# Kernel optimization log

Hardware: AMD Instinct MI355X
Metric: run time of the kernel (lower is better)

The kernel has to match this reference:

```python
import jax, jax.numpy as jnp
import numpy as np
import math

HIDDEN = 1024
HEADS = 16
HEAD_DIM = HIDDEN // HEADS


def setup_inputs() -> dict:
    key = jax.random.key(0)
    ks = jax.random.split(key, 9)
    s = 1.0 / math.sqrt(HIDDEN)
    x = jax.random.normal(ks[0], (4, 2048, HIDDEN), dtype=jnp.float32)
    Wq = jax.random.uniform(ks[1], (HIDDEN, HIDDEN), jnp.float32, -s, s)
    bq = jax.random.uniform(ks[2], (HIDDEN,), jnp.float32, -s, s)
    Wk = jax.random.uniform(ks[3], (HIDDEN, HIDDEN), jnp.float32, -s, s)
    bk = jax.random.uniform(ks[4], (HIDDEN,), jnp.float32, -s, s)
    Wv = jax.random.uniform(ks[5], (HIDDEN, HIDDEN), jnp.float32, -s, s)
    bv = jax.random.uniform(ks[6], (HIDDEN,), jnp.float32, -s, s)
    Wo = jax.random.uniform(ks[7], (HIDDEN, HIDDEN), jnp.float32, -s, s)
    bo = jax.random.uniform(ks[8], (HIDDEN,), jnp.float32, -s, s)
    return {"x": x, "Wq": Wq, "bq": bq, "Wk": Wk, "bk": bk,
            "Wv": Wv, "bv": bv, "Wo": Wo, "bo": bo}


def reference(x, Wq, bq, Wk, bk, Wv, bv, Wo, bo):
    B, T, D = x.shape
    H, Hd = HEADS, HEAD_DIM
    scale = 1.0 / math.sqrt(Hd)
    # projections (torch Linear: y = x @ W.T + b)
    q = (x @ Wq.T + bq).reshape(B, T, H, Hd).transpose(0, 2, 1, 3)  # [B,H,T,Hd]
    k = (x @ Wk.T + bk).reshape(B, T, H, Hd).transpose(0, 2, 1, 3)
    v = (x @ Wv.T + bv).reshape(B, T, H, Hd).transpose(0, 2, 1, 3)
    scores = jnp.einsum("bhqd,bhkd->bhqk", q, k) * scale  # [B,H,T,T]
    attn = jax.nn.softmax(scores, axis=-1)
    out = jnp.einsum("bhqk,bhkd->bhqd", attn, v)  # [B,H,T,Hd]
    out = out.transpose(0, 2, 1, 3).reshape(B, T, D)
    out = out @ Wo.T + bo
    return out.mean(axis=1)  # [B, D]
```

## Files before the change

kernel.cpp:

```cpp
#include <hip/hip_runtime.h>
#include <stdint.h>

#define HIDDEN 1024
#define HEADS 16
#define HEAD_DIM 64
#define BATCH 4
#define SEQ 2048
#define NTOK (BATCH * SEQ)

typedef __attribute__((ext_vector_type(8))) short bf16x8;
typedef __attribute__((ext_vector_type(4))) float floatx4;
typedef __attribute__((ext_vector_type(16))) float floatx16;

#define SCALE_Q 0.18033688011112042f

__device__ __forceinline__ unsigned short f2bf(float f) {
    union { float f; unsigned u; } x; x.f = f;
    unsigned r = x.u + 0x7fffu + ((x.u >> 16) & 1u);
    return (unsigned short)(r >> 16);
}

__device__ __forceinline__ float fast_exp2(float x) {
#if __has_builtin(__builtin_amdgcn_exp2f)
    return __builtin_amdgcn_exp2f(x);
#else
    return exp2f(x);
#endif
}

typedef __attribute__((address_space(3))) unsigned int lds_u32;
typedef const __attribute__((address_space(1))) unsigned int gl_u32;

__device__ __forceinline__ void async_cp16(const void* g, void* l) {
#if __has_builtin(__builtin_amdgcn_global_load_lds)
    __builtin_amdgcn_global_load_lds((gl_u32*)g, (lds_u32*)l, 16, 0, 0);
#else
    *(uint4*)((char*)l + (threadIdx.x & 63) * 16) = *(const uint4*)g;
#endif
}

__global__ __launch_bounds__(256) void conv_all(
    const float* __restrict__ x, const float* __restrict__ Wq,
    const float* __restrict__ Wk, const float* __restrict__ Wv,
    unsigned short* __restrict__ x_bf, unsigned short* __restrict__ wq_bf,
    unsigned short* __restrict__ wk_bf, unsigned short* __restrict__ wv_bf,
    float* __restrict__ accp) {
    const int blk = blockIdx.x, tid = threadIdx.x;
    const float* src;
    unsigned short* dst;
    size_t i;
    if (blk < 8192) {
        src = x; dst = x_bf; i = (size_t)blk * 256 + tid;
        if (blk < 16) accp[blk * 256 + tid] = 0.0f;
    } else {
        int r = blk - 8192;
        int s = r >> 10;
        src = (s == 0) ? Wq : (s == 1) ? Wk : Wv;
        dst = (s == 0) ? wq_bf : (s == 1) ? wk_bf : wv_bf;
        i = (size_t)(r & 1023) * 256 + tid;
    }
    float4 v = *(const float4*)(src + 4 * i);
    unsigned short o[4];
    o[0] = f2bf(v.x); o[1] = f2bf(v.y); o[2] = f2bf(v.z); o[3] = f2bf(v.w);
    *(ushort4*)(dst + 4 * i) = *(ushort4*)o;
}

__global__ __launch_bounds__(256, 2) void qkv_gemm(
    const unsigned short* __restrict__ X,
    const unsigned short* __restrict__ W0, const unsigned short* __restrict__ W1,
    const unsigned short* __restrict__ W2,
    const float* __restrict__ b0, const float* __restrict__ b1,
    const float* __restrict__ b2,
    unsigned short* __restrict__ O0, unsigned short* __restrict__ O1,
    unsigned short* __restrict__ O2) {
    __shared__ unsigned short Alds[2][4096];
    __shared__ unsigned short Blds[2][6144];

    const int id = blockIdx.x;
    const int mb = id & 63, nb = id >> 6;
    const int m0 = mb * 128, n0 = nb * 64;

    const int tid = threadIdx.x, lane = tid & 63, wave = tid >> 6;

    const unsigned short* WZ0 = W0;
    const unsigned short* WZ1 = W1;
    const unsigned short* WZ2 = W2;

    const unsigned short* ga[2];
#pragma unroll
    for (int j = 0; j < 2; ++j)
        ga[j] = X + (size_t)(m0 + wave * 32 + j * 16 + (lane >> 2)) * HIDDEN + (lane & 3) * 8;

    const unsigned short* gb[3];
    int bdst[3];
#pragma unroll
    for (int jj = 0; jj < 3; ++jj) {
        const int i = wave * 3 + jj;
        const int z = i >> 2, seg = i & 3;
        const unsigned short* Wz = (z == 0) ? WZ0 : (z == 1) ? WZ1 : WZ2;
        gb[jj] = Wz + (size_t)(n0 + seg * 16 + (lane >> 2)) * HIDDEN + (lane & 3) * 8;
        bdst[jj] = z * 4096 + seg * 1024;
    }

    floatx4 acc[3][2][4];
#pragma unroll
    for (int z = 0; z < 3; ++z)
#pragma unroll
        for (int tm = 0; tm < 2; ++tm)
#pragma unroll
            for (int tn = 0; tn < 4; ++tn)
#pragma unroll
                for (int r = 0; r < 4; ++r) acc[z][tm][tn][r] = 0.f;

#pragma unroll
    for (int j = 0; j < 2; ++j) {
        async_cp16(ga[j], (char*)Alds[0] + wave * 2048 + j * 1024);
        ga[j] += 32;
    }
#pragma unroll
    for (int jj = 0; jj < 3; ++jj) {
        async_cp16(gb[jj], (char*)Blds[0] + bdst[jj]);
        gb[jj] += 32;
    }
    __syncthreads();

    const int frag_off = (lane & 15) * 64 + (lane >> 4) * 16;
    for (int kt = 0; kt < 32; ++kt) {
        const int cur = kt & 1;
        if (kt < 31) {
#pragma unroll
            for (int j = 0; j < 2; ++j) {
                async_cp16(ga[j], (char*)Alds[cur ^ 1] + wave * 2048 + j * 1024);
                ga[j] += 32;
            }
#pragma unroll
            for (int jj = 0; jj < 3; ++jj) {
                async_cp16(gb[jj], (char*)Blds[cur ^ 1] + bdst[jj]);
                gb[jj] += 32;
            }
        }
        bf16x8 af[2];
#pragma unroll
        for (int tm = 0; tm < 2; ++tm)
            af[tm] = *(bf16x8*)((char*)Alds[cur] + (wave * 32 + tm * 16) * 64 + frag_off);
#pragma unroll
        for (int z = 0; z < 3; ++z) {
            bf16x8 bfr[4];
#pragma unroll
            for (int tn = 0; tn < 4; ++tn)
                bfr[tn] = *(bf16x8*)((char*)Blds[cur] + z * 4096 + tn * 1024 + frag_off);
#pragma unroll
            for (int tm = 0; tm < 2; ++tm)
#pragma unroll
                for (int tn = 0; tn < 4; ++tn)
                    acc[z][tm][tn] = __builtin_amdgcn_mfma_f32_16x16x32_bf16(af[tm], bfr[tn], acc[z][tm][tn], 0, 0, 0);
        }
        if (kt < 31) __syncthreads();
    }

    const int col = lane & 15, rbase = (lane >> 4) * 4;
#pragma unroll
    for (int z = 0; z < 3; ++z) {
        const float* bias = (z == 0) ? b0 : (z == 1) ? b1 : b2;
        unsigned short* O = (z == 0) ? O0 : (z == 1) ? O1 : O2;
        const float sc = (z == 0) ? SCALE_Q : 1.0f;
#pragma unroll
        for (int tm = 0; tm < 2; ++tm) {
#pragma unroll
            for (int tn = 0; tn < 4; ++tn) {
                const int n = n0 + tn * 16 + col;
                const float bs = bias[n];
                const int m_base = m0 + wave * 32 + tm * 16 + rbase;
                if (z == 2) {
                    const int hh = n >> 6, dd = n & 63;
                    const int bb = m_base >> 11, tt = m_base & (SEQ - 1);
                    const int tb = tt >> 7, gg = (tt & 127) >> 2;
                    const int gr = (gg + dd) & 31;
                    unsigned short vals[4];
#pragma unroll
                    for (int r = 0; r < 4; ++r) vals[r] = f2bf(acc[z][tm][tn][r] + bs);
                    *(ushort4*)&O[(((size_t)bb * HEADS + hh) * HEAD_DIM + dd) * SEQ + tb * 128 + gr * 4] =
                        *(ushort4*)vals;
                } else {
#pragma unroll
                    for (int r = 0; r < 4; ++r)
                        O[(size_t)(m_base + r) * HIDDEN + n] = f2bf((acc[z][tm][tn][r] + bs) * sc);
                }
            }
        }
    }
}

__global__ __launch_bounds__(256, 2) void attn_mfma(
    const unsigned short* __restrict__ Q, const unsigned short* __restrict__ K,
    const unsigned short* __restrict__ Vt, float* __restrict__ accp) {
    __shared__ unsigned short Klds[2][8192];
    __shared__ unsigned short Vlds[2][8192];

    const int tid = threadIdx.x, lane = tid & 63, wave = tid >> 6;
    const int lq = lane & 31, g2 = lane >> 5;

    const int f = blockIdx.x;
    const int bh = (f & 7) * 8 + ((f >> 3) & 7);
    const int qc = f >> 6;
    const int b = bh >> 4, h = bh & 15;

    bf16x8 qfrag[2][4];
#pragma unroll
    for (int g = 0; g < 2; ++g) {
        const size_t qb = ((size_t)(b * SEQ + qc * 256 + wave * 64 + g * 32 + lq)) * HIDDEN
                          + h * HEAD_DIM + g2 * 8;
#pragma unroll
        for (int ds = 0; ds < 4; ++ds) qfrag[g][ds] = *(const bf16x8*)&Q[qb + ds * 16];
    }

    const unsigned short* kg[4];
    const unsigned short* vg[4];
    {
        const int kr = lane >> 3;
        const int kc = ((lane & 7) ^ kr) * 8;
#pragma unroll
        for (int j = 0; j < 4; ++j)
            kg[j] = K + ((size_t)(b * SEQ + wave * 32 + j * 8 + kr)) * HIDDEN + h * HEAD_DIM + kc;
#pragma unroll
        for (int j = 0; j < 4; ++j) {
            const int dl = wave * 16 + j * 4 + (lane >> 4);
            vg[j] = Vt + ((size_t)bh * HEAD_DIM + dl) * SEQ + (lane & 15) * 8;
        }
    }

    floatx16 oacc[2][2], lacc[2];
#pragma unroll
    for (int g = 0; g < 2; ++g)
#pragma unroll
        for (int r = 0; r < 16; ++r) { oacc[g][0][r] = 0.f; oacc[g][1][r] = 0.f; lacc[g][r] = 0.f; }

    bf16x8 ones;
    {
        union { bf16x8 v; unsigned u[4]; } o;
        o.u[0] = o.u[1] = o.u[2] = o.u[3] = 0x3F803F80u;
        ones = o.v;
    }

#pragma unroll
    for (int j = 0; j < 4; ++j) {
        async_cp16(kg[j], (char*)Klds[0] + (wave * 32 + j * 8) * 128);
        async_cp16(vg[j], (char*)Vlds[0] + (wave * 16 + j * 4) * 256);
        kg[j] += 128 * HIDDEN; vg[j] += 128;
    }
    __syncthreads();

    for (int it = 0; it < 16; ++it) {
        const int cur = it & 1;
        if (it < 15) {
#pragma unroll
            for (int j = 0; j < 4; ++j) {
                async_cp16(kg[j], (char*)Klds[cur ^ 1] + (wave * 32 + j * 8) * 128);
                async_cp16(vg[j], (char*)Vlds[cur ^ 1] + (wave * 16 + j * 4) * 256);
                kg[j] += 128 * HIDDEN; vg[j] += 128;
            }
        }
#pragma unroll
        for (int ks4 = 0; ks4 < 4; ++ks4) {
            const int kk = ks4 * 32;
            const int rr = kk + lq;
            bf16x8 kf[4];
#pragma unroll
            for (int ds = 0; ds < 4; ++ds)
                kf[ds] = *(bf16x8*)((char*)Klds[cur] + rr * 128 + (((g2 + 2 * ds) ^ (lq & 7)) * 16));

            unsigned pk[2][8];
#pragma unroll
            for (int g = 0; g < 2; ++g) {
                floatx16 sacc;
#pragma unroll
                for (int r = 0; r < 16; ++r) sacc[r] = 0.f;
#pragma unroll
                for (int ds = 0; ds < 4; ++ds)
                    sacc = __builtin_amdgcn_mfma_f32_32x32x16_bf16(kf[ds], qfrag[g][ds], sacc, 0, 0, 0);
#pragma unroll
                for (int j = 0; j < 8; ++j) {
                    union { float f; unsigned u; } plo, phi;
                    plo.f = fast_exp2(sacc[2 * j]);
                    phi.f = fast_exp2(sacc[2 * j + 1]);
                    pk[g][j] = __builtin_amdgcn_perm(phi.u, plo.u, 0x07060302u);
                }
            }
#pragma unroll
            for (int ks2 = 0; ks2 < 2; ++ks2) {
                const int gran0 = 8 * ks4 + 4 * ks2 + g2;
                bf16x8 vf[2];
#pragma unroll
                for (int nf = 0; nf < 2; ++nf) {
                    const int d = nf * 32 + lq;
                    const int p0 = (gran0 + d) & 31;
                    const int p1 = (gran0 + 2 + d) & 31;
                    union { uint2 h[2]; bf16x8 v; } u;
                    u.h[0] = *(uint2*)((char*)Vlds[cur] + d * 256 + p0 * 8);
                    u.h[1] = *(uint2*)((char*)Vlds[cur] + d * 256 + p1 * 8);
                    vf[nf] = u.v;
                }
#pragma unroll
                for (int g = 0; g < 2; ++g) {
                    union { uint4 u; bf16x8 v; } af;
                    af.u.x = pk[g][4 * ks2];
                    af.u.y = pk[g][4 * ks2 + 1];
                    af.u.z = pk[g][4 * ks2 + 2];
                    af.u.w = pk[g][4 * ks2 + 3];
#pragma unroll
                    for (int nf = 0; nf < 2; ++nf)
                        oacc[g][nf] = __builtin_amdgcn_mfma_f32_32x32x16_bf16(af.v, vf[nf], oacc[g][nf], 0, 0, 0);
                    lacc[g] = __builtin_amdgcn_mfma_f32_32x32x16_bf16(af.v, ones, lacc[g], 0, 0, 0);
                }
            }
        }
        if (it < 15) __syncthreads();
    }

#pragma unroll
    for (int g = 0; g < 2; ++g)
#pragma unroll
        for (int nf = 0; nf < 2; ++nf) {
            float v = 0.f;
#pragma unroll
            for (int r = 0; r < 16; ++r) v += oacc[g][nf][r] / lacc[g][r];
            v += __shfl_xor(v, 32, 64);
            if (lane < 32)
                atomicAdd(&accp[b * HIDDEN + h * HEAD_DIM + nf * 32 + lq], v);
        }
}

__global__ __launch_bounds__(256) void out_proj(const float* __restrict__ acc,
                                                const float* __restrict__ Wo,
                                                const float* __restrict__ bo,
                                                float* __restrict__ out) {
    const int n = blockIdx.x * 256 + threadIdx.x;
    const int b = blockIdx.y;
    const float invT = 1.0f / (float)SEQ;
    float s = 0.f;
    for (int k = 0; k < HIDDEN; k += 4) {
        float4 w = *(const float4*)&Wo[(size_t)n * HIDDEN + k];
        float4 a = *(const float4*)&acc[b * HIDDEN + k];
        s += w.x * a.x + w.y * a.y + w.z * a.z + w.w * a.w;
    }
    out[b * HIDDEN + n] = s * invT + bo[n];
}

extern "C" void kernel_launch(void* const* d_in, const int* in_sizes, int n_in,
                              void* d_out, int out_size, void* d_ws, size_t ws_size,
                              hipStream_t stream) {
    const float* x  = (const float*)d_in[0];
    const float* Wq = (const float*)d_in[1];
    const float* bq = (const float*)d_in[2];
    const float* Wk = (const float*)d_in[3];
    const float* bk = (const float*)d_in[4];
    const float* Wv = (const float*)d_in[5];
    const float* bv = (const float*)d_in[6];
    const float* Wo = (const float*)d_in[7];
    const float* bo = (const float*)d_in[8];
    float* out = (float*)d_out;

    char* ws = (char*)d_ws;
    unsigned short* x_bf  = (unsigned short*)(ws);
    unsigned short* wq_bf = (unsigned short*)(ws + 16777216);
    unsigned short* wk_bf = (unsigned short*)(ws + 18874368);
    unsigned short* wv_bf = (unsigned short*)(ws + 20971520);
    unsigned short* q_bf  = (unsigned short*)(ws + 23068672);
    unsigned short* k_bf  = (unsigned short*)(ws + 39845888);
    unsigned short* vt_bf = (unsigned short*)(ws + 56623104);
    float*          accp  = (float*)(ws + 73400320);

    conv_all<<<dim3(8192 + 3072), dim3(256), 0, stream>>>(
        x, Wq, Wk, Wv, x_bf, wq_bf, wk_bf, wv_bf, accp);

    qkv_gemm<<<dim3(1024), dim3(256), 0, stream>>>(
        x_bf, wq_bf, wk_bf, wv_bf, bq, bk, bv, q_bf, k_bf, vt_bf);

    attn_mfma<<<dim3(512), dim3(256), 0, stream>>>(q_bf, k_bf, vt_bf, accp);

    out_proj<<<dim3(HIDDEN / 256, BATCH), dim3(256), 0, stream>>>(accp, Wo, bo, out);
}
```

Before: 269.3 us.

## Stage QKV epilogue through LDS, XOR-swizzle V layout, split-K out projection

The QKV GEMM epilogue now writes tiles into a shared-memory buffer and then emits coalesced 16-byte global stores for Q, K and the transposed V, replacing scattered 2-byte stores. The transposed-V storage swizzle changes from an additive rotation to an XOR scheme, and the attention kernel's LDS reads are updated to match. The out-projection GEMV is split over K across four waves with a shared-memory reduction, which gives 64 blocks instead of 16. The extra LDS (about 18KB) may lower occupancy of the GEMM, and the added barriers cost some time.

Result: faster. 252.4 us (-6.3%).

```diff
diff --git a/kernel.cpp b/kernel.cpp
--- a/kernel.cpp
+++ b/kernel.cpp
@@ -75,6 +75,7 @@
     unsigned short* __restrict__ O2) {
     __shared__ unsigned short Alds[2][4096];
     __shared__ unsigned short Blds[2][6144];
+    __shared__ __align__(16) unsigned short tbuf[9216];
 
     const int id = blockIdx.x;
     const int mb = id & 63, nb = id >> 6;
@@ -82,10 +83,6 @@
 
     const int tid = threadIdx.x, lane = tid & 63, wave = tid >> 6;
 
-    const unsigned short* WZ0 = W0;
-    const unsigned short* WZ1 = W1;
-    const unsigned short* WZ2 = W2;
-
     const unsigned short* ga[2];
 #pragma unroll
     for (int j = 0; j < 2; ++j)
@@ -97,7 +94,7 @@
     for (int jj = 0; jj < 3; ++jj) {
         const int i = wave * 3 + jj;
         const int z = i >> 2, seg = i & 3;
-        const unsigned short* Wz = (z == 0) ? WZ0 : (z == 1) ? WZ1 : WZ2;
+        const unsigned short* Wz = (z == 0) ? W0 : (z == 1) ? W1 : W2;
         gb[jj] = Wz + (size_t)(n0 + seg * 16 + (lane >> 2)) * HIDDEN + (lane & 3) * 8;
         bdst[jj] = z * 4096 + seg * 1024;
     }
@@ -162,31 +159,51 @@
 #pragma unroll
     for (int z = 0; z < 3; ++z) {
         const float* bias = (z == 0) ? b0 : (z == 1) ? b1 : b2;
-        unsigned short* O = (z == 0) ? O0 : (z == 1) ? O1 : O2;
         const float sc = (z == 0) ? SCALE_Q : 1.0f;
-#pragma unroll
-        for (int tm = 0; tm < 2; ++tm) {
-#pragma unroll
-            for (int tn = 0; tn < 4; ++tn) {
-                const int n = n0 + tn * 16 + col;
-                const float bs = bias[n];
-                const int m_base = m0 + wave * 32 + tm * 16 + rbase;
-                if (z == 2) {
-                    const int hh = n >> 6, dd = n & 63;
-                    const int bb = m_base >> 11, tt = m_base & (SEQ - 1);
-                    const int tb = tt >> 7, gg = (tt & 127) >> 2;
-                    const int gr = (gg + dd) & 31;
+        __syncthreads();
+        if (z == 2) {
+#pragma unroll
+            for (int tm = 0; tm < 2; ++tm)
+#pragma unroll
+                for (int tn = 0; tn < 4; ++tn) {
+                    const int nn = tn * 16 + col;
+                    const float bs = bias[n0 + nn];
+                    const int mi0 = wave * 32 + tm * 16 + rbase;
                     unsigned short vals[4];
 #pragma unroll
-                    for (int r = 0; r < 4; ++r) vals[r] = f2bf(acc[z][tm][tn][r] + bs);
-                    *(ushort4*)&O[(((size_t)bb * HEADS + hh) * HEAD_DIM + dd) * SEQ + tb * 128 + gr * 4] =
-                        *(ushort4*)vals;
-                } else {
+                    for (int r = 0; r < 4; ++r) vals[r] = f2bf(acc[2][tm][tn][r] + bs);
+                    *(ushort4*)&tbuf[nn * 136 + mi0] = *(ushort4*)vals;
+                }
+            __syncthreads();
+            const int dd = tid >> 2, part = tid & 3;
+            const int hh = n0 >> 6;
+            const int bb = m0 >> 11, tb = (m0 & (SEQ - 1)) >> 7;
+            unsigned short* dst = O2 + (((size_t)bb * HEADS + hh) * HEAD_DIM + dd) * SEQ
+                                     + tb * 128 + part * 32;
+            const unsigned short* srcl = &tbuf[dd * 136 + part * 32];
+#pragma unroll
+            for (int i = 0; i < 4; ++i)
+                *(uint4*)(dst + i * 8) = *(const uint4*)(srcl + i * 8);
+        } else {
+            unsigned short* O = (z == 0) ? O0 : O1;
+#pragma unroll
+            for (int tm = 0; tm < 2; ++tm)
+#pragma unroll
+                for (int tn = 0; tn < 4; ++tn) {
+                    const int nn = tn * 16 + col;
+                    const float bs = bias[n0 + nn];
+                    const int mi0 = wave * 32 + tm * 16 + rbase;
 #pragma unroll
                     for (int r = 0; r < 4; ++r)
-                        O[(size_t)(m_base + r) * HIDDEN + n] = f2bf((acc[z][tm][tn][r] + bs) * sc);
+                        tbuf[(mi0 + r) * 72 + nn] = f2bf((acc[z][tm][tn][r] + bs) * sc);
                 }
-            }
+            __syncthreads();
+            const int r = tid >> 1, half = tid & 1;
+            unsigned short* dst = O + (size_t)(m0 + r) * HIDDEN + n0 + half * 32;
+            const unsigned short* srcl = &tbuf[r * 72 + half * 32];
+#pragma unroll
+            for (int i = 0; i < 4; ++i)
+                *(uint4*)(dst + i * 8) = *(const uint4*)(srcl + i * 8);
         }
     }
 }
@@ -225,7 +242,8 @@
 #pragma unroll
         for (int j = 0; j < 4; ++j) {
             const int dl = wave * 16 + j * 4 + (lane >> 4);
-            vg[j] = Vt + ((size_t)bh * HEAD_DIM + dl) * SEQ + (lane & 15) * 8;
+            const int cc = ((lane & 15) ^ (dl & 15)) * 8;
+            vg[j] = Vt + ((size_t)bh * HEAD_DIM + dl) * SEQ + cc;
         }
     }
 
@@ -288,16 +306,15 @@
             }
 #pragma unroll
             for (int ks2 = 0; ks2 < 2; ++ks2) {
-                const int gran0 = 8 * ks4 + 4 * ks2 + g2;
                 bf16x8 vf[2];
 #pragma unroll
                 for (int nf = 0; nf < 2; ++nf) {
                     const int d = nf * 32 + lq;
-                    const int p0 = (gran0 + d) & 31;
-                    const int p1 = (gran0 + 2 + d) & 31;
+                    const int c0 = (4 * ks4 + 2 * ks2) ^ (d & 15);
+                    const int c1 = (4 * ks4 + 2 * ks2 + 1) ^ (d & 15);
                     union { uint2 h[2]; bf16x8 v; } u;
-                    u.h[0] = *(uint2*)((char*)Vlds[cur] + d * 256 + p0 * 8);
-                    u.h[1] = *(uint2*)((char*)Vlds[cur] + d * 256 + p1 * 8);
+                    u.h[0] = *(uint2*)((char*)Vlds[cur] + d * 256 + c0 * 16 + g2 * 8);
+                    u.h[1] = *(uint2*)((char*)Vlds[cur] + d * 256 + c1 * 16 + g2 * 8);
                     vf[nf] = u.v;
                 }
 #pragma unroll
@@ -334,16 +351,26 @@
                                                 const float* __restrict__ Wo,
                                                 const float* __restrict__ bo,
                                                 float* __restrict__ out) {
-    const int n = blockIdx.x * 256 + threadIdx.x;
+    __shared__ float red[256];
+    const int n = blockIdx.x * 64 + (threadIdx.x & 63);
+    const int ks = threadIdx.x >> 6;
     const int b = blockIdx.y;
-    const float invT = 1.0f / (float)SEQ;
+    const float* wr = Wo + (size_t)n * HIDDEN + ks * 256;
+    const float* ar = acc + b * HIDDEN + ks * 256;
     float s = 0.f;
-    for (int k = 0; k < HIDDEN; k += 4) {
-        float4 w = *(const float4*)&Wo[(size_t)n * HIDDEN + k];
-        float4 a = *(const float4*)&acc[b * HIDDEN + k];
+#pragma unroll 8
+    for (int k = 0; k < 256; k += 4) {
+        float4 w = *(const float4*)(wr + k);
+        float4 a = *(const float4*)(ar + k);
         s += w.x * a.x + w.y * a.y + w.z * a.z + w.w * a.w;
     }
-    out[b * HIDDEN + n] = s * invT + bo[n];
+    red[threadIdx.x] = s;
+    __syncthreads();
+    if (threadIdx.x < 64) {
+        float t = red[threadIdx.x] + red[threadIdx.x + 64]
+                + red[threadIdx.x + 128] + red[threadIdx.x + 192];
+        out[b * HIDDEN + n] = t * (1.0f / (float)SEQ) + bo[n];
+    }
 }
 
 extern "C" void kernel_launch(void* const* d_in, const int* in_sizes, int n_in,
@@ -378,5 +405,5 @@
 
     attn_mfma<<<dim3(512), dim3(256), 0, stream>>>(q_bf, k_bf, vt_bf, accp);
 
-    out_proj<<<dim3(HIDDEN / 256, BATCH), dim3(256), 0, stream>>>(accp, Wo, bo, out);
-}
+    out_proj<<<dim3(16, BATCH), dim3(256), 0, stream>>>(accp, Wo, bo, out);
+}
```
